# Performance work log

Hardware: AMD Instinct MI355X
Metric: run time of the kernel (lower is better)

## Reference

```python
import jax, jax.numpy as jnp
import numpy as np

D_MODEL = 256
N_HEADS = 8
N_LEVELS = 3
N_POINTS = 4
HEAD_DIM = D_MODEL // N_HEADS
SPATIAL_SHAPES = [(80, 80), (40, 40), (20, 20)]
B = 16
LEN_Q = 300
N_TOTAL = sum(h * w for h, w in SPATIAL_SHAPES)  # 8400
N_LP = N_LEVELS * N_POINTS


def setup_inputs() -> dict:
    key = jax.random.key(0)
    ks = jax.random.split(key, 8)
    s = 0.02
    return {
        "query": jax.random.normal(ks[0], (B, LEN_Q, D_MODEL), jnp.float32),
        "reference_points": jax.random.uniform(ks[1], (B, LEN_Q, N_LEVELS, 2), jnp.float32),
        "input_flatten": jax.random.normal(ks[2], (B, N_TOTAL, D_MODEL), jnp.float32),
        "W_off": jax.random.normal(ks[3], (D_MODEL, N_HEADS * N_LP * 2), jnp.float32) * s,
        "b_off": jnp.zeros((N_HEADS * N_LP * 2,), jnp.float32),
        "W_attn": jax.random.normal(ks[4], (D_MODEL, N_HEADS * N_LP), jnp.float32) * s,
        "b_attn": jnp.zeros((N_HEADS * N_LP,), jnp.float32),
        "W_val": jax.random.normal(ks[5], (D_MODEL, D_MODEL), jnp.float32) * s,
        "b_val": jnp.zeros((D_MODEL,), jnp.float32),
        "W_out": jax.random.normal(ks[6], (D_MODEL, D_MODEL), jnp.float32) * s,
        "b_out": jnp.zeros((D_MODEL,), jnp.float32),
    }


def _ms_deform_core(value, sampling_locations, attention_weights):
    # value: (B, n_heads, head_dim, N_total); locations: (B, Lq, H, L, P, 2) in [0,1]
    Bq, Lq = sampling_locations.shape[0], sampling_locations.shape[1]
    BN = Bq * N_HEADS
    grids = 2.0 * sampling_locations - 1.0
    starts = np.cumsum([0] + [h * w for h, w in SPATIAL_SHAPES])
    sampled_levels = []
    for lid, (H, W) in enumerate(SPATIAL_SHAPES):
        val_l = value[..., starts[lid]:starts[lid + 1]]                    # (B,H,hd,HW)
        val_flat = val_l.reshape(BN, HEAD_DIM, H * W).transpose(0, 2, 1)   # (BN,HW,hd)
        g = grids[:, :, :, lid].transpose(0, 2, 1, 3, 4).reshape(BN, Lq, N_POINTS, 2)
        ix = ((g[..., 0] + 1.0) * W - 1.0) / 2.0
        iy = ((g[..., 1] + 1.0) * H - 1.0) / 2.0
        ix0 = jnp.floor(ix).astype(jnp.int32)
        iy0 = jnp.floor(iy).astype(jnp.int32)
        ix1 = ix0 + 1
        iy1 = iy0 + 1
        fx = (ix - ix0.astype(ix.dtype))[..., None]
        fy = (iy - iy0.astype(iy.dtype))[..., None]

        def corner(iyc, ixc):
            valid = ((ixc >= 0) & (ixc < W) & (iyc >= 0) & (iyc < H)).astype(val_flat.dtype)
            idx = (jnp.clip(iyc, 0, H - 1) * W + jnp.clip(ixc, 0, W - 1))
            idx = idx.reshape(BN, Lq * N_POINTS, 1)
            v = jnp.take_along_axis(val_flat, idx, axis=1)
            return v.reshape(BN, Lq, N_POINTS, HEAD_DIM) * valid[..., None]

        v00 = corner(iy0, ix0)
        v01 = corner(iy0, ix1)
        v10 = corner(iy1, ix0)
        v11 = corner(iy1, ix1)
        sampled = ((1 - fx) * (1 - fy)) * v00 + (fx * (1 - fy)) * v01 \
                + ((1 - fx) * fy) * v10 + (fx * fy) * v11
        sampled_levels.append(sampled.transpose(0, 3, 1, 2))               # (BN,hd,Lq,P)
    sv = jnp.stack(sampled_levels, axis=-2).reshape(BN, HEAD_DIM, Lq, N_LP)
    a = attention_weights.transpose(0, 2, 1, 3).reshape(BN, 1, Lq, N_LP)
    out = jnp.sum(sv * a, axis=-1)                                         # (BN,hd,Lq)
    return out.reshape(Bq, D_MODEL, Lq).transpose(0, 2, 1)                 # (B,Lq,D)


def reference(query, reference_points, input_flatten,
              W_off, b_off, W_attn, b_attn, W_val, b_val, W_out, b_out):
    Bq, Lq = query.shape[0], query.shape[1]
    value = input_flatten @ W_val + b_val
    value = value.reshape(Bq, -1, N_HEADS, HEAD_DIM).transpose(0, 2, 3, 1)  # (B,H,hd,N)
    off = (query @ W_off + b_off).reshape(Bq, Lq, N_HEADS, N_LEVELS, N_POINTS, 2)
    attn = jax.nn.softmax((query @ W_attn + b_attn).reshape(Bq, Lq, N_HEADS, N_LP), axis=-1)
    # offset normalizer is (W,H) per level (x first)
    norm = jnp.array([[w, h] for h, w in SPATIAL_SHAPES], jnp.float32)
    loc = reference_points[:, :, None, :, None, :] + off / norm[None, None, None, :, None, :]
    out = _ms_deform_core(value, loc, attn)
    return out @ W_out + b_out
```

## Files before the change

### kernel.cpp

```cpp
#include <hip/hip_runtime.h>
#include <hip/hip_bf16.h>

#define DM 256
#define NH 8
#define HD 32
#define NLV 3
#define NPT 4
#define NLP 12
#define BB 16
#define LQ 300
#define NT 8400
#define MROWS (BB * NT)
#define QROWS (BB * LQ)
#define KP 40
#define KP2 72

typedef __bf16 bf16x8 __attribute__((ext_vector_type(8)));
typedef __bf16 bf16x4 __attribute__((ext_vector_type(4)));
typedef float  f32x16 __attribute__((ext_vector_type(16)));

__global__ void k_wt(const float* __restrict__ W_val,
                     const float* __restrict__ W_off,
                     const float* __restrict__ W_attn,
                     const float* __restrict__ W_out,
                     __hip_bfloat16* __restrict__ Wf,
                     __hip_bfloat16* __restrict__ Wt2,
                     __hip_bfloat16* __restrict__ Wt3)
{
    const int n = blockIdx.x;
    const int k = threadIdx.x;
    if (n < 256) {
        Wf[(size_t)(k >> 3) * 2048 + n * 8 + (k & 7)] =
            __float2bfloat16(W_val[(size_t)k * 256 + n]);
    } else if (n < 544) {
        const int n2 = n - 256;
        float v = (n2 < 192) ? W_off[(size_t)k * 192 + n2]
                             : W_attn[(size_t)k * 96 + (n2 - 192)];
        Wt2[(size_t)(k >> 5) * 9216 + n2 * 32 + (k & 31)] = __float2bfloat16(v);
    } else {
        const int n3 = n - 544;
        Wt3[(size_t)(k >> 5) * 8192 + n3 * 32 + (k & 31)] =
            __float2bfloat16(W_out[(size_t)k * 256 + n3]);
    }
}

__global__ __launch_bounds__(256) void k_valproj(
    const float* __restrict__ A,
    const __hip_bfloat16* __restrict__ Wf,
    const float* __restrict__ bias,
    __hip_bfloat16* __restrict__ V)
{
    __shared__ __hip_bfloat16 As[2][32 * KP2];

    const int t    = threadIdx.x;
    const int m0   = blockIdx.x * 32;
    const int wave = t >> 6;
    const int lane = t & 63;
    const int lm   = lane & 31;
    const int kh   = lane >> 5;
    const int lk   = kh * 8;

    f32x16 acc[2];
#pragma unroll
    for (int j = 0; j < 2; j++)
#pragma unroll
        for (int e = 0; e < 16; e++) acc[j][e] = 0.f;

    const int ar = t >> 3;
    const int ak = (t & 7) * 8;

    const __hip_bfloat16* wf0 = Wf + (size_t)(wave * 64 + lm) * 8 + kh * 2048;

    {
        const float* ap = A + (size_t)(m0 + ar) * 256 + ak;
        float4 a0 = *(const float4*)ap;
        float4 a1 = *(const float4*)(ap + 4);
        union { __hip_bfloat162 h2[4]; bf16x8 v; } ua;
        ua.h2[0] = __float22bfloat162_rn(make_float2(a0.x, a0.y));
        ua.h2[1] = __float22bfloat162_rn(make_float2(a0.z, a0.w));
        ua.h2[2] = __float22bfloat162_rn(make_float2(a1.x, a1.y));
        ua.h2[3] = __float22bfloat162_rn(make_float2(a1.z, a1.w));
        *(bf16x8*)(&As[0][ar * KP2 + ak]) = ua.v;
    }
    __syncthreads();

#pragma unroll
    for (int it = 0; it < 4; ++it) {
        const int buf = it & 1;
        float4 na0, na1;
        if (it < 3) {
            const float* ap = A + (size_t)(m0 + ar) * 256 + (it + 1) * 64 + ak;
            na0 = *(const float4*)ap;
            na1 = *(const float4*)(ap + 4);
        }
#pragma unroll
        for (int ks = 0; ks < 4; ++ks) {
            const int g = it * 4 + ks;
            bf16x8 af = *(const bf16x8*)(&As[buf][lm * KP2 + ks * 16 + lk]);
            bf16x8 b0 = *(const bf16x8*)(wf0 + (size_t)g * 4096);
            bf16x8 b1 = *(const bf16x8*)(wf0 + (size_t)g * 4096 + 256);
            acc[0] = __builtin_amdgcn_mfma_f32_32x32x16_bf16(af, b0, acc[0], 0, 0, 0);
            acc[1] = __builtin_amdgcn_mfma_f32_32x32x16_bf16(af, b1, acc[1], 0, 0, 0);
        }
        if (it < 3) {
            union { __hip_bfloat162 h2[4]; bf16x8 v; } ua;
            ua.h2[0] = __float22bfloat162_rn(make_float2(na0.x, na0.y));
            ua.h2[1] = __float22bfloat162_rn(make_float2(na0.z, na0.w));
            ua.h2[2] = __float22bfloat162_rn(make_float2(na1.x, na1.y));
            ua.h2[3] = __float22bfloat162_rn(make_float2(na1.z, na1.w));
            *(bf16x8*)(&As[buf ^ 1][ar * KP2 + ak]) = ua.v;
            __syncthreads();
        }
    }

#pragma unroll
    for (int j = 0; j < 2; j++) {
        const int n  = wave * 64 + j * 32 + lm;
        const float bn = bias[n];
        const int h  = n >> 5;
        const int d  = n & 31;
#pragma unroll
        for (int r = 0; r < 16; r++) {
            int rl = (r & 3) + 8 * (r >> 2) + 4 * kh;
            int m  = m0 + rl;
            int b  = m / NT;
            int pos = m - b * NT;
            V[((size_t)(b * NH + h) * NT + pos) * HD + d] =
                __float2bfloat16(acc[j][r] + bn);
        }
    }
}

__global__ __launch_bounds__(192) void k_offattn(
    const float* __restrict__ Q,
    const __hip_bfloat16* __restrict__ Wt2,
    const float* __restrict__ boff,
    const float* __restrict__ battn,
    float* __restrict__ off_out,
    float* __restrict__ attn_out)
{
    __shared__ __hip_bfloat16 As[32 * KP];
    __shared__ __hip_bfloat16 Ws[288 * KP];

    const int t    = threadIdx.x;
    const int m0   = blockIdx.x * 32;
    const int wave = t >> 6;
    const int lane = t & 63;
    const int lm   = lane & 31;
    const int lk   = (lane >> 5) * 8;

    f32x16 acc[3];
#pragma unroll
    for (int j = 0; j < 3; j++)
#pragma unroll
        for (int e = 0; e < 16; e++) acc[j][e] = 0.f;

    for (int kt = 0; kt < 256; kt += 32) {
        if (t < 128) {
            const int ar = t >> 2;
            const int ak = (t & 3) * 8;
            const float* ap = Q + (size_t)(m0 + ar) * 256 + kt + ak;
            float4 a0 = *(const float4*)ap;
            float4 a1 = *(const float4*)(ap + 4);
            union { __hip_bfloat162 h2[4]; bf16x8 v; } ua;
            ua.h2[0] = __float22bfloat162_rn(make_float2(a0.x, a0.y));
            ua.h2[1] = __float22bfloat162_rn(make_float2(a0.z, a0.w));
            ua.h2[2] = __float22bfloat162_rn(make_float2(a1.x, a1.y));
            ua.h2[3] = __float22bfloat162_rn(make_float2(a1.z, a1.w));
            *(bf16x8*)(As + ar * KP + ak) = ua.v;
        }
        {
            const __hip_bfloat16* wp = Wt2 + (size_t)(kt >> 5) * 9216 + t * 32;
            __hip_bfloat16* wd = Ws + t * KP;
            *(bf16x8*)(wd + 0)  = *(const bf16x8*)(wp + 0);
            *(bf16x8*)(wd + 8)  = *(const bf16x8*)(wp + 8);
            *(bf16x8*)(wd + 16) = *(const bf16x8*)(wp + 16);
            *(bf16x8*)(wd + 24) = *(const bf16x8*)(wp + 24);
            if (t < 96) {
                const __hip_bfloat16* wp2 = Wt2 + (size_t)(kt >> 5) * 9216 + (t + 192) * 32;
                __hip_bfloat16* wd2 = Ws + (t + 192) * KP;
                *(bf16x8*)(wd2 + 0)  = *(const bf16x8*)(wp2 + 0);
                *(bf16x8*)(wd2 + 8)  = *(const bf16x8*)(wp2 + 8);
                *(bf16x8*)(wd2 + 16) = *(const bf16x8*)(wp2 + 16);
                *(bf16x8*)(wd2 + 24) = *(const bf16x8*)(wp2 + 24);
            }
        }
        __syncthreads();

#pragma unroll
        for (int kk = 0; kk < 32; kk += 16) {
            bf16x8 af = *(const bf16x8*)(As + lm * KP + kk + lk);
#pragma unroll
            for (int j = 0; j < 3; j++) {
                bf16x8 bf = *(const bf16x8*)(Ws + (wave * 96 + j * 32 + lm) * KP + kk + lk);
                acc[j] = __builtin_amdgcn_mfma_f32_32x32x16_bf16(af, bf, acc[j], 0, 0, 0);
            }
        }
        __syncthreads();
    }

#pragma unroll
    for (int j = 0; j < 3; j++) {
        const int n = wave * 96 + j * 32 + lm;
        const float bias_ = (n < 192) ? boff[n] : battn[n - 192];
#pragma unroll
        for (int r = 0; r < 16; r++) {
            int rl = (r & 3) + 8 * (r >> 2) + 4 * (lane >> 5);
            int m  = m0 + rl;
            float v = acc[j][r] + bias_;
            if (n < 192) off_out[(size_t)m * 192 + n] = v;
            else         attn_out[(size_t)m * 96 + (n - 192)] = v;
        }
    }
}

__global__ __launch_bounds__(256) void k_sample(
    const float* __restrict__ off_raw,
    const float* __restrict__ attn_raw,
    const float* __restrict__ refp,
    const __hip_bfloat16* __restrict__ V,
    __hip_bfloat16* __restrict__ sampled)
{
    const int t  = threadIdx.x;
    const int q2 = t >> 7;
    const int tq = t & 127;
    const int bq = blockIdx.x * 2 + q2;
    const int b  = bq / LQ;

    __shared__ float aw[2][96];
    __shared__ float wc[2][96][4];
    __shared__ int   ic[2][96][4];

    if (tq < 8) {
        float v[12];
        float mx = -1e30f;
#pragma unroll
        for (int i = 0; i < 12; i++) {
            v[i] = attn_raw[(size_t)bq * 96 + tq * 12 + i];
            mx = fmaxf(mx, v[i]);
        }
        float s = 0.f;
#pragma unroll
        for (int i = 0; i < 12; i++) { v[i] = expf(v[i] - mx); s += v[i]; }
        float inv = 1.f / s;
#pragma unroll
        for (int i = 0; i < 12; i++) aw[q2][tq * 12 + i] = v[i] * inv;
    }
    __syncthreads();

    if (tq < 96) {
        const float dims[3]  = {80.f, 40.f, 20.f};
        const int startsl[3] = {0, 6400, 8000};
        const int idiml[3]   = {80, 40, 20};
        int h = tq / 12, lp = tq - h * 12, l = lp >> 2, p = lp & 3;
        float ox = off_raw[(size_t)bq * 192 + ((h * 3 + l) * 4 + p) * 2 + 0];
        float oy = off_raw[(size_t)bq * 192 + ((h * 3 + l) * 4 + p) * 2 + 1];
        float rx = refp[(size_t)bq * 6 + l * 2 + 0];
        float ry = refp[(size_t)bq * 6 + l * 2 + 1];
        float D  = dims[l];
        float lx = rx + ox / D;
        float ly = ry + oy / D;
        float ix = lx * D - 0.5f;
        float iy = ly * D - 0.5f;
        const int Dl = idiml[l];
        const int st = startsl[l];

        float fix = floorf(ix), fiy = floorf(iy);
        int ix0 = (int)fix, iy0 = (int)fiy;
        int ix1 = ix0 + 1, iy1 = iy0 + 1;
        float fx = ix - fix, fy = iy - fiy;

        float mx0 = (ix0 >= 0 && ix0 < Dl) ? 1.f : 0.f;
        float mx1 = (ix1 >= 0 && ix1 < Dl) ? 1.f : 0.f;
        float my0 = (iy0 >= 0 && iy0 < Dl) ? 1.f : 0.f;
        float my1 = (iy1 >= 0 && iy1 < Dl) ? 1.f : 0.f;

        int cx0 = min(max(ix0, 0), Dl - 1);
        int cx1 = min(max(ix1, 0), Dl - 1);
        int cy0 = min(max(iy0, 0), Dl - 1);
        int cy1 = min(max(iy1, 0), Dl - 1);

        float a = aw[q2][tq];
        wc[q2][tq][0] = (1.f - fx) * (1.f - fy) * mx0 * my0 * a;
        wc[q2][tq][1] = fx * (1.f - fy) * mx1 * my0 * a;
        wc[q2][tq][2] = (1.f - fx) * fy * mx0 * my1 * a;
        wc[q2][tq][3] = fx * fy * mx1 * my1 * a;
        ic[q2][tq][0] = (st + cy0 * Dl + cx0) * HD;
        ic[q2][tq][1] = (st + cy0 * Dl + cx1) * HD;
        ic[q2][tq][2] = (st + cy1 * Dl + cx0) * HD;
        ic[q2][tq][3] = (st + cy1 * Dl + cx1) * HD;
    }
    __syncthreads();

    const int h  = tq >> 4;
    const int dp = (tq & 15) * 2;
    const __hip_bfloat16* vb = V + (size_t)(b * NH + h) * NT * HD + dp;

    float acc0 = 0.f, acc1 = 0.f;
#pragma unroll
    for (int lp = 0; lp < 12; lp++) {
        const int s = h * 12 + lp;
        float4 w4 = *(const float4*)(&wc[q2][s][0]);
        int4   i4 = *(const int4*)(&ic[q2][s][0]);
        float2 v00 = __bfloat1622float2(*(const __hip_bfloat162*)(vb + i4.x));
        float2 v01 = __bfloat1622float2(*(const __hip_bfloat162*)(vb + i4.y));
        float2 v10 = __bfloat1622float2(*(const __hip_bfloat162*)(vb + i4.z));
        float2 v11 = __bfloat1622float2(*(const __hip_bfloat162*)(vb + i4.w));
        acc0 = fmaf(w4.x, v00.x, fmaf(w4.y, v01.x, fmaf(w4.z, v10.x, fmaf(w4.w, v11.x, acc0))));
        acc1 = fmaf(w4.x, v00.y, fmaf(w4.y, v01.y, fmaf(w4.z, v10.y, fmaf(w4.w, v11.y, acc1))));
    }
    *(__hip_bfloat162*)(sampled + (size_t)bq * 256 + h * 32 + dp) =
        __float22bfloat162_rn(make_float2(acc0, acc1));
}

__global__ __launch_bounds__(256) void k_outproj(
    const __hip_bfloat16* __restrict__ A,
    const __hip_bfloat16* __restrict__ Wt3,
    const float* __restrict__ bias,
    float* __restrict__ out)
{
    __shared__ __hip_bfloat16 As[32 * KP];
    __shared__ __hip_bfloat16 Ws[256 * KP];

    const int t    = threadIdx.x;
    const int m0   = blockIdx.x * 32;
    const int wave = t >> 6;
    const int lane = t & 63;
    const int lm   = lane & 31;
    const int lk   = (lane >> 5) * 8;

    f32x16 acc[2];
#pragma unroll
    for (int j = 0; j < 2; j++)
#pragma unroll
        for (int e = 0; e < 16; e++) acc[j][e] = 0.f;

    const int ar = t >> 3;
    const int ak = (t & 7) * 4;

    for (int kt = 0; kt < 256; kt += 32) {
        *(bf16x4*)(As + ar * KP + ak) =
            *(const bf16x4*)(A + (size_t)(m0 + ar) * 256 + kt + ak);
        {
            const __hip_bfloat16* wp = Wt3 + (size_t)(kt >> 5) * 8192 + t * 32;
            __hip_bfloat16* wd = Ws + t * KP;
            *(bf16x8*)(wd + 0)  = *(const bf16x8*)(wp + 0);
            *(bf16x8*)(wd + 8)  = *(const bf16x8*)(wp + 8);
            *(bf16x8*)(wd + 16) = *(const bf16x8*)(wp + 16);
            *(bf16x8*)(wd + 24) = *(const bf16x8*)(wp + 24);
        }
        __syncthreads();

#pragma unroll
        for (int kk = 0; kk < 32; kk += 16) {
            bf16x8 af = *(const bf16x8*)(As + lm * KP + kk + lk);
            bf16x8 bf0 = *(const bf16x8*)(Ws + (wave * 64 + 0 * 32 + lm) * KP + kk + lk);
            bf16x8 bf1 = *(const bf16x8*)(Ws + (wave * 64 + 1 * 32 + lm) * KP + kk + lk);
            acc[0] = __builtin_amdgcn_mfma_f32_32x32x16_bf16(af, bf0, acc[0], 0, 0, 0);
            acc[1] = __builtin_amdgcn_mfma_f32_32x32x16_bf16(af, bf1, acc[1], 0, 0, 0);
        }
        __syncthreads();
    }

#pragma unroll
    for (int j = 0; j < 2; j++) {
        const int n = wave * 64 + j * 32 + lm;
        const float bn = bias[n];
#pragma unroll
        for (int r = 0; r < 16; r++) {
            int rl = (r & 3) + 8 * (r >> 2) + 4 * (lane >> 5);
            int m  = m0 + rl;
            out[(size_t)m * 256 + n] = acc[j][r] + bn;
        }
    }
}

extern "C" void kernel_launch(void* const* d_in, const int* in_sizes, int n_in,
                              void* d_out, int out_size, void* d_ws, size_t ws_size,
                              hipStream_t stream) {
    const float* query  = (const float*)d_in[0];
    const float* refp   = (const float*)d_in[1];
    const float* inputf = (const float*)d_in[2];
    const float* W_off  = (const float*)d_in[3];
    const float* b_off  = (const float*)d_in[4];
    const float* W_attn = (const float*)d_in[5];
    const float* b_attn = (const float*)d_in[6];
    const float* W_val  = (const float*)d_in[7];
    const float* b_val  = (const float*)d_in[8];
    const float* W_out  = (const float*)d_in[9];
    const float* b_out  = (const float*)d_in[10];
    float* out = (float*)d_out;

    char* ws = (char*)d_ws;
    __hip_bfloat16* value   = (__hip_bfloat16*)ws;
    float* off_raw          = (float*)(ws + 68812800);
    float* attn_raw         = (float*)(ws + 72499200);
    __hip_bfloat16* sampled = (__hip_bfloat16*)(ws + 74342400);
    __hip_bfloat16* Wf      = (__hip_bfloat16*)(ws + 76800000);
    __hip_bfloat16* Wt2     = (__hip_bfloat16*)(ws + 76931072);
    __hip_bfloat16* Wt3     = (__hip_bfloat16*)(ws + 77078528);

    k_wt<<<800, 256, 0, stream>>>(W_val, W_off, W_attn, W_out, Wf, Wt2, Wt3);
    k_valproj<<<MROWS / 32, 256, 0, stream>>>(inputf, Wf, b_val, value);
    k_offattn<<<QROWS / 32, 192, 0, stream>>>(query, Wt2, b_off, b_attn,
                                              off_raw, attn_raw);
    k_sample<<<QROWS / 2, 256, 0, stream>>>(off_raw, attn_raw, refp, value, sampled);
    k_outproj<<<QROWS / 32, 256, 0, stream>>>(sampled, Wt3, b_out, out);
}
```

Before: 279.2 us.

## Swap MFMA operands for row-contiguous vector epilogue stores; widen sampling per thread

The three GEMM kernels swap the A/B operands of the MFMA so each lane holds consecutive output columns of one row. The epilogues can then add bias with float4 loads and write 4-wide vector stores, replacing scattered scalar stores with per-row index math. The sampling kernel now handles four queries per block, each thread gathering four bf16 channels per corner instead of two, which halves the number of gather instructions. This changes the thread mapping in all four kernels and makes the sampling kernel more sensitive to register use.

```diff
diff --git a/kernel.cpp b/kernel.cpp
--- a/kernel.cpp
+++ b/kernel.cpp
@@ -99,8 +99,8 @@
             bf16x8 af = *(const bf16x8*)(&As[buf][lm * KP2 + ks * 16 + lk]);
             bf16x8 b0 = *(const bf16x8*)(wf0 + (size_t)g * 4096);
             bf16x8 b1 = *(const bf16x8*)(wf0 + (size_t)g * 4096 + 256);
-            acc[0] = __builtin_amdgcn_mfma_f32_32x32x16_bf16(af, b0, acc[0], 0, 0, 0);
-            acc[1] = __builtin_amdgcn_mfma_f32_32x32x16_bf16(af, b1, acc[1], 0, 0, 0);
+            acc[0] = __builtin_amdgcn_mfma_f32_32x32x16_bf16(b0, af, acc[0], 0, 0, 0);
+            acc[1] = __builtin_amdgcn_mfma_f32_32x32x16_bf16(b1, af, acc[1], 0, 0, 0);
         }
         if (it < 3) {
             union { __hip_bfloat162 h2[4]; bf16x8 v; } ua;
@@ -113,20 +113,24 @@
         }
     }
 
+    const int m   = m0 + lm;
+    const int b   = m / NT;
+    const int pos = m - b * NT;
 #pragma unroll
     for (int j = 0; j < 2; j++) {
-        const int n  = wave * 64 + j * 32 + lm;
-        const float bn = bias[n];
-        const int h  = n >> 5;
-        const int d  = n & 31;
-#pragma unroll
-        for (int r = 0; r < 16; r++) {
-            int rl = (r & 3) + 8 * (r >> 2) + 4 * kh;
-            int m  = m0 + rl;
-            int b  = m / NT;
-            int pos = m - b * NT;
-            V[((size_t)(b * NH + h) * NT + pos) * HD + d] =
-                __float2bfloat16(acc[j][r] + bn);
+        const int h = wave * 2 + j;
+        __hip_bfloat16* vrow = V + ((size_t)(b * NH + h) * NT + pos) * HD;
+#pragma unroll
+        for (int g = 0; g < 4; g++) {
+            const int d0 = g * 8 + kh * 4;
+            const int n0 = wave * 64 + j * 32 + d0;
+            float4 b4 = *(const float4*)(bias + n0);
+            union { __hip_bfloat162 h2[2]; bf16x4 v; } u;
+            u.h2[0] = __float22bfloat162_rn(
+                make_float2(acc[j][g * 4 + 0] + b4.x, acc[j][g * 4 + 1] + b4.y));
+            u.h2[1] = __float22bfloat162_rn(
+                make_float2(acc[j][g * 4 + 2] + b4.z, acc[j][g * 4 + 3] + b4.w));
+            *(bf16x4*)(vrow + d0) = u.v;
         }
     }
 }
@@ -147,7 +151,8 @@
     const int wave = t >> 6;
     const int lane = t & 63;
     const int lm   = lane & 31;
-    const int lk   = (lane >> 5) * 8;
+    const int kh   = lane >> 5;
+    const int lk   = kh * 8;
 
     f32x16 acc[3];
 #pragma unroll
@@ -193,23 +198,35 @@
 #pragma unroll
             for (int j = 0; j < 3; j++) {
                 bf16x8 bf = *(const bf16x8*)(Ws + (wave * 96 + j * 32 + lm) * KP + kk + lk);
-                acc[j] = __builtin_amdgcn_mfma_f32_32x32x16_bf16(af, bf, acc[j], 0, 0, 0);
+                acc[j] = __builtin_amdgcn_mfma_f32_32x32x16_bf16(bf, af, acc[j], 0, 0, 0);
             }
         }
         __syncthreads();
     }
 
+    const int m = m0 + lm;
 #pragma unroll
     for (int j = 0; j < 3; j++) {
-        const int n = wave * 96 + j * 32 + lm;
-        const float bias_ = (n < 192) ? boff[n] : battn[n - 192];
-#pragma unroll
-        for (int r = 0; r < 16; r++) {
-            int rl = (r & 3) + 8 * (r >> 2) + 4 * (lane >> 5);
-            int m  = m0 + rl;
-            float v = acc[j][r] + bias_;
-            if (n < 192) off_out[(size_t)m * 192 + n] = v;
-            else         attn_out[(size_t)m * 96 + (n - 192)] = v;
+        const int nt_ = wave * 96 + j * 32;
+#pragma unroll
+        for (int g = 0; g < 4; g++) {
+            const int n0 = nt_ + g * 8 + kh * 4;
+            float4 o;
+            if (nt_ < 192) {
+                float4 b4 = *(const float4*)(boff + n0);
+                o.x = acc[j][g * 4 + 0] + b4.x;
+                o.y = acc[j][g * 4 + 1] + b4.y;
+                o.z = acc[j][g * 4 + 2] + b4.z;
+                o.w = acc[j][g * 4 + 3] + b4.w;
+                *(float4*)(off_out + (size_t)m * 192 + n0) = o;
+            } else {
+                float4 b4 = *(const float4*)(battn + n0 - 192);
+                o.x = acc[j][g * 4 + 0] + b4.x;
+                o.y = acc[j][g * 4 + 1] + b4.y;
+                o.z = acc[j][g * 4 + 2] + b4.z;
+                o.w = acc[j][g * 4 + 3] + b4.w;
+                *(float4*)(attn_out + (size_t)m * 96 + n0 - 192) = o;
+            }
         }
     }
 }
@@ -222,14 +239,14 @@
     __hip_bfloat16* __restrict__ sampled)
 {
     const int t  = threadIdx.x;
-    const int q2 = t >> 7;
-    const int tq = t & 127;
-    const int bq = blockIdx.x * 2 + q2;
+    const int q4 = t >> 6;
+    const int tq = t & 63;
+    const int bq = blockIdx.x * 4 + q4;
     const int b  = bq / LQ;
 
-    __shared__ float aw[2][96];
-    __shared__ float wc[2][96][4];
-    __shared__ int   ic[2][96][4];
+    __shared__ float aw[4][96];
+    __shared__ float wc[4][96][4];
+    __shared__ int   ic[4][96][4];
 
     if (tq < 8) {
         float v[12];
@@ -244,15 +261,16 @@
         for (int i = 0; i < 12; i++) { v[i] = expf(v[i] - mx); s += v[i]; }
         float inv = 1.f / s;
 #pragma unroll
-        for (int i = 0; i < 12; i++) aw[q2][tq * 12 + i] = v[i] * inv;
+        for (int i = 0; i < 12; i++) aw[q4][tq * 12 + i] = v[i] * inv;
     }
     __syncthreads();
 
-    if (tq < 96) {
+#pragma unroll
+    for (int pp = tq; pp < 96; pp += 64) {
         const float dims[3]  = {80.f, 40.f, 20.f};
         const int startsl[3] = {0, 6400, 8000};
         const int idiml[3]   = {80, 40, 20};
-        int h = tq / 12, lp = tq - h * 12, l = lp >> 2, p = lp & 3;
+        int h = pp / 12, lp = pp - h * 12, l = lp >> 2, p = lp & 3;
         float ox = off_raw[(size_t)bq * 192 + ((h * 3 + l) * 4 + p) * 2 + 0];
         float oy = off_raw[(size_t)bq * 192 + ((h * 3 + l) * 4 + p) * 2 + 1];
         float rx = refp[(size_t)bq * 6 + l * 2 + 0];
@@ -280,37 +298,46 @@
         int cy0 = min(max(iy0, 0), Dl - 1);
         int cy1 = min(max(iy1, 0), Dl - 1);
 
-        float a = aw[q2][tq];
-        wc[q2][tq][0] = (1.f - fx) * (1.f - fy) * mx0 * my0 * a;
-        wc[q2][tq][1] = fx * (1.f - fy) * mx1 * my0 * a;
-        wc[q2][tq][2] = (1.f - fx) * fy * mx0 * my1 * a;
-        wc[q2][tq][3] = fx * fy * mx1 * my1 * a;
-        ic[q2][tq][0] = (st + cy0 * Dl + cx0) * HD;
-        ic[q2][tq][1] = (st + cy0 * Dl + cx1) * HD;
-        ic[q2][tq][2] = (st + cy1 * Dl + cx0) * HD;
-        ic[q2][tq][3] = (st + cy1 * Dl + cx1) * HD;
+        float a = aw[q4][pp];
+        wc[q4][pp][0] = (1.f - fx) * (1.f - fy) * mx0 * my0 * a;
+        wc[q4][pp][1] = fx * (1.f - fy) * mx1 * my0 * a;
+        wc[q4][pp][2] = (1.f - fx) * fy * mx0 * my1 * a;
+        wc[q4][pp][3] = fx * fy * mx1 * my1 * a;
+        ic[q4][pp][0] = (st + cy0 * Dl + cx0) * HD;
+        ic[q4][pp][1] = (st + cy0 * Dl + cx1) * HD;
+        ic[q4][pp][2] = (st + cy1 * Dl + cx0) * HD;
+        ic[q4][pp][3] = (st + cy1 * Dl + cx1) * HD;
     }
     __syncthreads();
 
-    const int h  = tq >> 4;
-    const int dp = (tq & 15) * 2;
-    const __hip_bfloat16* vb = V + (size_t)(b * NH + h) * NT * HD + dp;
-
-    float acc0 = 0.f, acc1 = 0.f;
+    const int h  = tq >> 3;
+    const int dq = (tq & 7) * 4;
+    const __hip_bfloat16* vb = V + (size_t)(b * NH + h) * NT * HD + dq;
+
+    float a0 = 0.f, a1 = 0.f, a2 = 0.f, a3 = 0.f;
 #pragma unroll
     for (int lp = 0; lp < 12; lp++) {
         const int s = h * 12 + lp;
-        float4 w4 = *(const float4*)(&wc[q2][s][0]);
-        int4   i4 = *(const int4*)(&ic[q2][s][0]);
-        float2 v00 = __bfloat1622float2(*(const __hip_bfloat162*)(vb + i4.x));
-        float2 v01 = __bfloat1622float2(*(const __hip_bfloat162*)(vb + i4.y));
-        float2 v10 = __bfloat1622float2(*(const __hip_bfloat162*)(vb + i4.z));
-        float2 v11 = __bfloat1622float2(*(const __hip_bfloat162*)(vb + i4.w));
-        acc0 = fmaf(w4.x, v00.x, fmaf(w4.y, v01.x, fmaf(w4.z, v10.x, fmaf(w4.w, v11.x, acc0))));
-        acc1 = fmaf(w4.x, v00.y, fmaf(w4.y, v01.y, fmaf(w4.z, v10.y, fmaf(w4.w, v11.y, acc1))));
-    }
-    *(__hip_bfloat162*)(sampled + (size_t)bq * 256 + h * 32 + dp) =
-        __float22bfloat162_rn(make_float2(acc0, acc1));
+        float4 w4 = *(const float4*)(&wc[q4][s][0]);
+        int4   i4 = *(const int4*)(&ic[q4][s][0]);
+        union { bf16x4 v; __hip_bfloat162 h2[2]; } c00, c01, c10, c11;
+        c00.v = *(const bf16x4*)(vb + i4.x);
+        c01.v = *(const bf16x4*)(vb + i4.y);
+        c10.v = *(const bf16x4*)(vb + i4.z);
+        c11.v = *(const bf16x4*)(vb + i4.w);
+        float2 f00a = __bfloat1622float2(c00.h2[0]), f00b = __bfloat1622float2(c00.h2[1]);
+        float2 f01a = __bfloat1622float2(c01.h2[0]), f01b = __bfloat1622float2(c01.h2[1]);
+        float2 f10a = __bfloat1622float2(c10.h2[0]), f10b = __bfloat1622float2(c10.h2[1]);
+        float2 f11a = __bfloat1622float2(c11.h2[0]), f11b = __bfloat1622float2(c11.h2[1]);
+        a0 = fmaf(w4.x, f00a.x, fmaf(w4.y, f01a.x, fmaf(w4.z, f10a.x, fmaf(w4.w, f11a.x, a0))));
+        a1 = fmaf(w4.x, f00a.y, fmaf(w4.y, f01a.y, fmaf(w4.z, f10a.y, fmaf(w4.w, f11a.y, a1))));
+        a2 = fmaf(w4.x, f00b.x, fmaf(w4.y, f01b.x, fmaf(w4.z, f10b.x, fmaf(w4.w, f11b.x, a2))));
+        a3 = fmaf(w4.x, f00b.y, fmaf(w4.y, f01b.y, fmaf(w4.z, f10b.y, fmaf(w4.w, f11b.y, a3))));
+    }
+    union { bf16x4 v; __hip_bfloat162 h2[2]; } uo;
+    uo.h2[0] = __float22bfloat162_rn(make_float2(a0, a1));
+    uo.h2[1] = __float22bfloat162_rn(make_float2(a2, a3));
+    *(bf16x4*)(sampled + (size_t)bq * 256 + h * 32 + dq) = uo.v;
 }
 
 __global__ __launch_bounds__(256) void k_outproj(
@@ -327,7 +354,8 @@
     const int wave = t >> 6;
     const int lane = t & 63;
     const int lm   = lane & 31;
-    const int lk   = (lane >> 5) * 8;
+    const int kh   = lane >> 5;
+    const int lk   = kh * 8;
 
     f32x16 acc[2];
 #pragma unroll
@@ -356,21 +384,26 @@
             bf16x8 af = *(const bf16x8*)(As + lm * KP + kk + lk);
             bf16x8 bf0 = *(const bf16x8*)(Ws + (wave * 64 + 0 * 32 + lm) * KP + kk + lk);
             bf16x8 bf1 = *(const bf16x8*)(Ws + (wave * 64 + 1 * 32 + lm) * KP + kk + lk);
-            acc[0] = __builtin_amdgcn_mfma_f32_32x32x16_bf16(af, bf0, acc[0], 0, 0, 0);
-            acc[1] = __builtin_amdgcn_mfma_f32_32x32x16_bf16(af, bf1, acc[1], 0, 0, 0);
+            acc[0] = __builtin_amdgcn_mfma_f32_32x32x16_bf16(bf0, af, acc[0], 0, 0, 0);
+            acc[1] = __builtin_amdgcn_mfma_f32_32x32x16_bf16(bf1, af, acc[1], 0, 0, 0);
         }
         __syncthreads();
     }
 
+    const int m = m0 + lm;
+    float* orow = out + (size_t)m * 256;
 #pragma unroll
     for (int j = 0; j < 2; j++) {
-        const int n = wave * 64 + j * 32 + lm;
-        const float bn = bias[n];
-#pragma unroll
-        for (int r = 0; r < 16; r++) {
-            int rl = (r & 3) + 8 * (r >> 2) + 4 * (lane >> 5);
-            int m  = m0 + rl;
-            out[(size_t)m * 256 + n] = acc[j][r] + bn;
+#pragma unroll
+        for (int g = 0; g < 4; g++) {
+            const int n0 = wave * 64 + j * 32 + g * 8 + kh * 4;
+            float4 b4 = *(const float4*)(bias + n0);
+            float4 o;
+            o.x = acc[j][g * 4 + 0] + b4.x;
+            o.y = acc[j][g * 4 + 1] + b4.y;
+            o.z = acc[j][g * 4 + 2] + b4.z;
+            o.w = acc[j][g * 4 + 3] + b4.w;
+            *(float4*)(orow + n0) = o;
         }
     }
 }
@@ -404,6 +437,6 @@
     k_valproj<<<MROWS / 32, 256, 0, stream>>>(inputf, Wf, b_val, value);
     k_offattn<<<QROWS / 32, 192, 0, stream>>>(query, Wt2, b_off, b_attn,
                                               off_raw, attn_raw);
-    k_sample<<<QROWS / 2, 256, 0, stream>>>(off_raw, attn_raw, refp, value, sampled);
+    k_sample<<<QROWS / 4, 256, 0, stream>>>(off_raw, attn_raw, refp, value, sampled);
     k_outproj<<<QROWS / 32, 256, 0, stream>>>(sampled, Wt3, b_out, out);
 }
```

Measured after the change: 284.8 us. Within noise of the previous version (+2.0%).
